# Optimization experiments

Hardware: AMD Instinct MI355X
Metric: run time of the kernel (lower is better)

## Reference

```python
import jax, jax.numpy as jnp
import numpy as np

BS, N1, N2, D = 2, 512, 512, 64  # in_dim = out_dim = D
TEMP = 1.0
EPS = 1e-5
POOL_RATIO = 0.5


def setup_inputs() -> dict:
    key = jax.random.key(0)
    ks = iter(jax.random.split(key, 32))
    nrm = lambda shape, s=0.05: jax.random.normal(next(ks), shape, dtype=jnp.float32) * s
    inp = {
        "x1": jax.random.normal(next(ks), (BS, N1, D), dtype=jnp.float32),
        "x2": jax.random.normal(next(ks), (BS, N2, D), dtype=jnp.float32),
        # proj_type1 / proj_type2 (Linear in->in); weights stored [in, out]
        "W1": nrm((D, D)), "b1": jnp.zeros((D,), jnp.float32),
        "W2": nrm((D, D)), "b2": jnp.zeros((D,), jnp.float32),
        # att_proj / att_projM (Linear in->out)
        "Wa": nrm((D, D)), "ba": jnp.zeros((D,), jnp.float32),
        "WaM": nrm((D, D)), "baM": jnp.zeros((D,), jnp.float32),
        # attention weight vectors (out_dim, 1)
        "w11": nrm((D, 1), 0.2), "w22": nrm((D, 1), 0.2),
        "w12": nrm((D, 1), 0.2), "wM": nrm((D, 1), 0.2),
        # projections
        "Wpa": nrm((D, D)), "bpa": jnp.zeros((D,), jnp.float32),
        "Wwoa": nrm((D, D)), "bwoa": jnp.zeros((D,), jnp.float32),
        "WpaM": nrm((D, D)), "bpaM": jnp.zeros((D,), jnp.float32),
        "WwoaM": nrm((D, D)), "bwoaM": jnp.zeros((D,), jnp.float32),
        # BatchNorm1d affine params
        "gamma": jnp.ones((D,), jnp.float32), "beta": jnp.zeros((D,), jnp.float32),
        # GraphPool score layer (Linear D->1), shared pool as in Model
        "Wp": nrm((D, 1), 0.2), "bp": jnp.zeros((1,), jnp.float32),
    }
    return inp


def _htrg_gat(x1, x2, W1, b1, W2, b2, Wa, ba, WaM, baM, w11, w22, w12, wM,
              Wpa, bpa, Wwoa, bwoa, WpaM, bpaM, WwoaM, bwoaM, gamma, beta):
    n1 = x1.shape[1]
    x1p = x1 @ W1 + b1
    x2p = x2 @ W2 + b2
    x = jnp.concatenate([x1p, x2p], axis=1)          # (b, N, d)
    master = jnp.mean(x, axis=1, keepdims=True)       # (b, 1, d)

    # --- attention map: pairwise node products, blockwise score weights ---
    pair = x[:, :, None, :] * x[:, None, :, :]        # (b, N, N, d)
    t = jnp.tanh(pair @ Wa + ba)                      # (b, N, N, d)
    top = jnp.concatenate([t[:, :n1, :n1] @ w11, t[:, :n1, n1:] @ w12], axis=2)
    bot = jnp.concatenate([t[:, n1:, :n1] @ w12, t[:, n1:, n1:] @ w22], axis=2)
    board = jnp.concatenate([top, bot], axis=1) / TEMP  # (b, N, N, 1)
    att = jax.nn.softmax(board, axis=-2)

    # --- master update ---
    tm = jnp.tanh((x * master) @ WaM + baM)           # (b, N, d)
    am = jax.nn.softmax((tm @ wM) / TEMP, axis=-2)    # (b, N, 1)
    agg_m = jnp.einsum('bn,bnd->bd', am[..., 0], x)[:, None, :]  # (b, 1, d)
    master_new = (agg_m @ WpaM + bpaM) + (master @ WwoaM + bwoaM)

    # --- project nodes with attention ---
    agg = jnp.einsum('bij,bjd->bid', att[..., 0], x)  # (b, N, d)
    xo = (agg @ Wpa + bpa) + (x @ Wwoa + bwoa)

    # --- BatchNorm1d over flattened (b*N) rows, then SELU ---
    mu = jnp.mean(xo, axis=(0, 1))
    var = jnp.var(xo, axis=(0, 1))
    xo = (xo - mu) * jax.lax.rsqrt(var + EPS) * gamma + beta
    xo = jax.nn.selu(xo)
    return xo[:, :n1], xo[:, n1:], master_new


def _graph_pool(x, Wp, bp):
    # scores -> sigmoid -> scale features -> top-k gather
    n = x.shape[1]
    k = max(int(n * POOL_RATIO), 1)
    scores = jax.nn.sigmoid(x @ Wp + bp)              # (b, n, 1)
    _, idx = jax.lax.top_k(scores[..., 0], k)         # (b, k)
    xs = x * scores
    return jnp.take_along_axis(xs, idx[..., None], axis=1)  # (b, k, d)


def reference(x1, x2, W1, b1, W2, b2, Wa, ba, WaM, baM, w11, w22, w12, wM,
              Wpa, bpa, Wwoa, bwoa, WpaM, bpaM, WwoaM, bwoaM, gamma, beta, Wp, bp):
    o1, o2, master = _htrg_gat(x1, x2, W1, b1, W2, b2, Wa, ba, WaM, baM,
                               w11, w22, w12, wM, Wpa, bpa, Wwoa, bwoa,
                               WpaM, bpaM, WwoaM, bwoaM, gamma, beta)
    p1 = _graph_pool(o1, Wp, bp)
    p2 = _graph_pool(o2, Wp, bp)
    return jnp.concatenate([p1, p2], axis=1)          # (b, n1/2 + n2/2, d)
```

## Files before the change

### kernel.cpp

```cpp
#include <hip/hip_runtime.h>

typedef float f32x4 __attribute__((ext_vector_type(4)));
typedef short short8 __attribute__((ext_vector_type(8)));

#define N_TOT 1024
#define N_HALF 512
#define D 64
#define KPOOL 256

#if __has_builtin(__builtin_amdgcn_exp2f)
#define EXP2F(x) __builtin_amdgcn_exp2f(x)
#else
#define EXP2F(x) __expf((x) * 0.6931471805599453f)
#endif
#if __has_builtin(__builtin_amdgcn_rcpf)
#define RCPF(x) __builtin_amdgcn_rcpf(x)
#else
#define RCPF(x) (1.0f / (x))
#endif

__device__ __forceinline__ short f2bf(float v) {
    unsigned u = __float_as_uint(v);
    u += 0x7FFFu + ((u >> 16) & 1u);
    return (short)(u >> 16);
}
__device__ __forceinline__ float bf2f(unsigned short u) {
    return __uint_as_float(((unsigned)u) << 16);
}

__global__ void k_proj(const float* __restrict__ x1, const float* __restrict__ x2,
                       const float* __restrict__ W1, const float* __restrict__ b1,
                       const float* __restrict__ W2, const float* __restrict__ b2,
                       float* __restrict__ x_f, unsigned short* __restrict__ x_bf,
                       unsigned short* __restrict__ xT_hi, unsigned short* __restrict__ xT_lo) {
    int r = blockIdx.x;
    int b = r >> 10, n = r & 1023;
    const float *src, *W, *bias;
    if (n < N_HALF) { src = x1 + (b * N_HALF + n) * D;            W = W1; bias = b1; }
    else            { src = x2 + (b * N_HALF + (n - N_HALF)) * D; W = W2; bias = b2; }
    __shared__ float row[D];
    int t = threadIdx.x;
    row[t] = src[t];
    __syncthreads();
    float acc = bias[t];
#pragma unroll
    for (int d = 0; d < D; ++d) acc = fmaf(row[d], W[d * D + t], acc);
    unsigned short hi = (unsigned short)f2bf(acc);
    unsigned short lo = (unsigned short)f2bf(acc - bf2f(hi));
    x_f[r * D + t] = acc;
    x_bf[r * D + t] = hi;
    xT_hi[((size_t)b * D + t) * N_TOT + n] = hi;
    xT_lo[((size_t)b * D + t) * N_TOT + n] = lo;
}

__global__ void __launch_bounds__(256)
k_score(const float* __restrict__ x_f, const unsigned short* __restrict__ x_bf,
        const float* __restrict__ Wa, const float* __restrict__ ba,
        const float* __restrict__ w11, const float* __restrict__ w22,
        const float* __restrict__ w12, unsigned* __restrict__ Ep) {
    int bid = blockIdx.x;
    int b = (bid >= 2560) ? 1 : 0;
    int m = bid - b * 2560;
    int i, c0;
    if (m < 1024)      { i = m >> 2;                        c0 = m & 3; }
    else if (m < 1792) { int t = m - 1024; i = 256 + t / 3; c0 = t % 3; }
    else if (m < 2304) { int t = m - 1792; i = 512 + (t >> 1); c0 = t & 1; }
    else               { i = 768 + (m - 2304);              c0 = 0; }
    int jt0 = i >> 4;
    int jts = jt0 + (c0 << 4);
    int jte = (jts + 16 < 64) ? (jts + 16) : 64;

    int tid = threadIdx.x;
    int l = tid & 63, wv = tid >> 6;
    int kc = l & 15, dg = l >> 4;

    __shared__ float xi_s[D];
    if (tid < D) xi_s[tid] = x_f[(b * N_TOT + i) * D + tid];
    __syncthreads();

    const float C2 = 2.885390081777927f;
    const float LOG2E = 1.4426950408889634f;

    const float* wTop = (i < N_HALF) ? w11 : w12;
    const float* wBot = (i < N_HALF) ? w12 : w22;

    short8 bfrag[4][2];
    float bac[4], wm2A[4], wm2B[4];
    float wsumA = 0.f, wsumB = 0.f;
#pragma unroll
    for (int kt = 0; kt < 4; ++kt) {
        int kcol = kt * 16 + kc;
        bac[kt] = ba[kcol] * C2;
        float wA = wTop[kcol], wB = wBot[kcol];
        wm2A[kt] = -2.f * wA; wm2B[kt] = -2.f * wB;
        wsumA += wA; wsumB += wB;
#pragma unroll
        for (int mm = 0; mm < 2; ++mm) {
            short8 f;
#pragma unroll
            for (int e = 0; e < 8; ++e) {
                int d = mm * 32 + dg * 8 + e;
                f[e] = f2bf(xi_s[d] * Wa[d * D + kcol]);
            }
            bfrag[kt][mm] = f;
        }
    }

    const unsigned short* xb_b = x_bf + b * N_TOT * D;
    unsigned* Eb = Ep + ((size_t)b << 20);
    for (int jt = jts + wv; jt < jte; jt += 4) {
        const unsigned short* arow = xb_b + (jt * 16 + kc) * D + dg * 8;
        short8 a0 = *reinterpret_cast<const short8*>(arow);
        short8 a1 = *reinterpret_cast<const short8*>(arow + 32);
        f32x4 acc[4];
#pragma unroll
        for (int kt = 0; kt < 4; ++kt) {
            f32x4 z = {0.f, 0.f, 0.f, 0.f};
            z = __builtin_amdgcn_mfma_f32_16x16x32_bf16(a0, bfrag[kt][0], z, 0, 0, 0);
            z = __builtin_amdgcn_mfma_f32_16x16x32_bf16(a1, bfrag[kt][1], z, 0, 0, 0);
            acc[kt] = z;
        }
        bool top = (jt < 32);
        float wsum_t = top ? wsumA : wsumB;
#pragma unroll
        for (int r = 0; r < 4; ++r) {
            float part = wsum_t;
#pragma unroll
            for (int kt = 0; kt < 4; ++kt) {
                float e2 = EXP2F(fmaf(acc[kt][r], C2, bac[kt]));
                float rcv = RCPF(e2 + 1.f);
                part = fmaf(top ? wm2A[kt] : wm2B[kt], rcv, part);
            }
            part += __shfl_xor(part, 1);
            part += __shfl_xor(part, 2);
            part += __shfl_xor(part, 4);
            part += __shfl_xor(part, 8);
            if (kc == 0) {
                int j = jt * 16 + dg * 4 + r;
                if (j >= i) {
                    float e = EXP2F(part * LOG2E);
                    unsigned short eh = (unsigned short)f2bf(e);
                    unsigned short el = (unsigned short)f2bf(e - bf2f(eh));
                    unsigned pk = ((unsigned)eh << 16) | (unsigned)el;
                    Eb[(size_t)i * N_TOT + j] = pk;
                    if (j > i) Eb[(size_t)j * N_TOT + i] = pk;
                }
            }
        }
    }
}

__global__ void __launch_bounds__(256)
k_aggp(const unsigned* __restrict__ Ep,
       const unsigned short* __restrict__ xT_hi, const unsigned short* __restrict__ xT_lo,
       float* __restrict__ pagg, float* __restrict__ rowsum_part) {
    int blk = blockIdx.x;
    int b = blk >> 7, rest = blk & 127;
    int it = rest >> 1, jh = rest & 1;
    int i0 = it * 16, jbase = jh * 512;
    int tid = threadIdx.x;
    int l = tid & 63, wv = tid >> 6;
    int kc = l & 15, dg = l >> 4;

    const unsigned* Eb = Ep + ((size_t)b << 20);
    const unsigned short* xTH = xT_hi + (size_t)b * D * N_TOT;
    const unsigned short* xTL = xT_lo + (size_t)b * D * N_TOT;

    f32x4 C0 = {0.f, 0.f, 0.f, 0.f}, C1 = C0, C2v = C0;
    const unsigned* Ap = Eb + (size_t)(i0 + kc) * N_TOT + jbase + dg * 8;
    const unsigned short* BH = xTH + (size_t)(wv * 16 + kc) * N_TOT + jbase + dg * 8;
    const unsigned short* BL = xTL + (size_t)(wv * 16 + kc) * N_TOT + jbase + dg * 8;
#pragma unroll 4
    for (int ks = 0; ks < 16; ++ks) {
        uint4 p0 = *reinterpret_cast<const uint4*>(Ap + ks * 32);
        uint4 p1 = *reinterpret_cast<const uint4*>(Ap + ks * 32 + 4);
        short8 ah, al;
        ah[0] = (short)(p0.x >> 16); al[0] = (short)(p0.x & 0xffff);
        ah[1] = (short)(p0.y >> 16); al[1] = (short)(p0.y & 0xffff);
        ah[2] = (short)(p0.z >> 16); al[2] = (short)(p0.z & 0xffff);
        ah[3] = (short)(p0.w >> 16); al[3] = (short)(p0.w & 0xffff);
        ah[4] = (short)(p1.x >> 16); al[4] = (short)(p1.x & 0xffff);
        ah[5] = (short)(p1.y >> 16); al[5] = (short)(p1.y & 0xffff);
        ah[6] = (short)(p1.z >> 16); al[6] = (short)(p1.z & 0xffff);
        ah[7] = (short)(p1.w >> 16); al[7] = (short)(p1.w & 0xffff);
        short8 bh = *reinterpret_cast<const short8*>(BH + ks * 32);
        short8 bl = *reinterpret_cast<const short8*>(BL + ks * 32);
        C0 = __builtin_amdgcn_mfma_f32_16x16x32_bf16(ah, bh, C0, 0, 0, 0);
        C1 = __builtin_amdgcn_mfma_f32_16x16x32_bf16(ah, bl, C1, 0, 0, 0);
        C2v = __builtin_amdgcn_mfma_f32_16x16x32_bf16(al, bh, C2v, 0, 0, 0);
    }
    f32x4 C = (C0 + C1) + C2v;

    {
        int row = wv * 4 + (l & 3);
        int seg = l >> 2;
        const unsigned* Er = Eb + (size_t)(i0 + row) * N_TOT + jbase + seg * 32;
        float rs = 0.f;
#pragma unroll
        for (int u = 0; u < 8; ++u) {
            uint4 v = *reinterpret_cast<const uint4*>(Er + u * 4);
            rs += __uint_as_float(v.x & 0xffff0000u) + __uint_as_float(v.x << 16);
            rs += __uint_as_float(v.y & 0xffff0000u) + __uint_as_float(v.y << 16);
            rs += __uint_as_float(v.z & 0xffff0000u) + __uint_as_float(v.z << 16);
            rs += __uint_as_float(v.w & 0xffff0000u) + __uint_as_float(v.w << 16);
        }
        rs += __shfl_xor(rs, 4);
        rs += __shfl_xor(rs, 8);
        rs += __shfl_xor(rs, 16);
        rs += __shfl_xor(rs, 32);
        if ((l & 3) == (l >> 2) % 4 && l < 4)
            ;
        if (l < 4) rowsum_part[(size_t)(b * 2 + jh) * N_TOT + i0 + wv * 4 + l] = rs;
    }

#pragma unroll
    for (int r = 0; r < 4; ++r)
        pagg[((size_t)(b * 2 + jh) * N_TOT + i0 + dg * 4 + r) * D + wv * 16 + kc] = C[r];
}

__global__ void __launch_bounds__(256)
k_aggfin(const float* __restrict__ pagg, const float* __restrict__ rowsum_part,
         const float* __restrict__ x_f,
         const float* __restrict__ Wpa, const float* __restrict__ bpa,
         const float* __restrict__ Wwoa, const float* __restrict__ bwoa,
         float* __restrict__ xo_pre, float* __restrict__ partials) {
    int b = blockIdx.x >> 6, it = blockIdx.x & 63;
    int i0 = it * 16;
    int tid = threadIdx.x;
    int l = tid & 63, wv = tid >> 6;

    __shared__ float aggL[16][D];
    __shared__ float xiL[16][D];
    __shared__ float xoL[16][D];
    __shared__ float riL[16];

    const float* p0 = pagg + ((size_t)(b * 2 + 0) * N_TOT + i0) * D;
    const float* p1 = pagg + ((size_t)(b * 2 + 1) * N_TOT + i0) * D;
    const float* xB = x_f + ((size_t)b * N_TOT + i0) * D;
#pragma unroll
    for (int u = 0; u < 4; ++u) {
        int idx = tid + u * 256;
        reinterpret_cast<float*>(aggL)[idx] = p0[idx] + p1[idx];
        reinterpret_cast<float*>(xiL)[idx] = xB[idx];
    }
    if (tid < 16)
        riL[tid] = 1.f / (rowsum_part[(size_t)(b * 2 + 0) * N_TOT + i0 + tid] +
                          rowsum_part[(size_t)(b * 2 + 1) * N_TOT + i0 + tid]);
    __syncthreads();
#pragma unroll
    for (int u = 0; u < 4; ++u) {
        int idx = tid + u * 256;
        reinterpret_cast<float*>(aggL)[idx] *= riL[idx >> 6];
    }
    __syncthreads();

    int k = l;
    float xo[4];
#pragma unroll
    for (int r = 0; r < 4; ++r) xo[r] = bpa[k] + bwoa[k];
    for (int dd = 0; dd < D; ++dd) {
        float wp = Wpa[dd * D + k], ww = Wwoa[dd * D + k];
#pragma unroll
        for (int r = 0; r < 4; ++r) {
            int row = wv * 4 + r;
            xo[r] += aggL[row][dd] * wp + xiL[row][dd] * ww;
        }
    }
#pragma unroll
    for (int r = 0; r < 4; ++r) {
        int row = wv * 4 + r;
        xo_pre[((size_t)b * N_TOT + i0 + row) * D + k] = xo[r];
        xoL[row][k] = xo[r];
    }
    __syncthreads();
    if (tid < D) {
        float s = 0.f, q = 0.f;
#pragma unroll
        for (int mm = 0; mm < 16; ++mm) { float v = xoL[mm][tid]; s += v; q = fmaf(v, v, q); }
        partials[blockIdx.x * 128 + tid] = s;
        partials[blockIdx.x * 128 + 64 + tid] = q;
    }
}

__global__ void k_stats2(const float* __restrict__ partials, float* __restrict__ stats) {
    int t = threadIdx.x;
    int g = t >> 7;
    int f128 = t & 127;
    float s = 0.f;
    for (int blk = g * 32; blk < g * 32 + 32; ++blk) s += partials[blk * 128 + f128];
    __shared__ float SQ[4][128];
    SQ[g][f128] = s;
    __syncthreads();
    if (t < 128) {
        float tot = SQ[0][t] + SQ[1][t] + SQ[2][t] + SQ[3][t];
        SQ[0][t] = tot;
    }
    __syncthreads();
    if (t < D) {
        float mu = SQ[0][t] * (1.f / 2048.f);
        float ex2 = SQ[0][64 + t] * (1.f / 2048.f);
        stats[t] = mu;
        stats[D + t] = rsqrtf(ex2 - mu * mu + 1e-5f);
    }
}

__global__ void k_norm(const float* __restrict__ xo_pre, const float* __restrict__ stats,
                       const float* __restrict__ gamma, const float* __restrict__ beta,
                       const float* __restrict__ Wp, const float* __restrict__ bp,
                       float* __restrict__ o_norm, float* __restrict__ scores) {
    int r = blockIdx.x * 4 + (threadIdx.x >> 6);
    int t = threadIdx.x & 63;
    float v = xo_pre[r * D + t];
    v = (v - stats[t]) * stats[D + t] * gamma[t] + beta[t];
    const float kScale = 1.0507009873554805f, kAlpha = 1.6732632423543772f;
    v = (v > 0.f) ? kScale * v : kScale * kAlpha * expm1f(v);
    o_norm[r * D + t] = v;
    float pd = v * Wp[t];
#pragma unroll
    for (int off = 32; off >= 1; off >>= 1) pd += __shfl_xor(pd, off);
    if (t == 0) scores[r] = 1.f / (1.f + __expf(-(pd + bp[0])));
}

__global__ void __launch_bounds__(512)
k_pool(const float* __restrict__ o_norm, const float* __restrict__ scores,
       float* __restrict__ out) {
    int b = blockIdx.x >> 1, half = blockIdx.x & 1;
    int tid = threadIdx.x;
    __shared__ float sc_s[N_HALF];
    __shared__ unsigned long long keys[N_HALF];
    __shared__ unsigned short map[KPOOL];

    {
        float sc = scores[b * N_TOT + half * N_HALF + tid];
        sc_s[tid] = sc;
        keys[tid] = ((unsigned long long)__float_as_uint(sc) << 10) | (unsigned)(511 - tid);
    }
    __syncthreads();
    unsigned long long mine = keys[tid];
    int cnt = 0;
#pragma unroll 8
    for (int qq = 0; qq < N_HALF; ++qq) cnt += (keys[qq] > mine) ? 1 : 0;
    if (cnt < KPOOL) map[cnt] = (unsigned short)tid;
    __syncthreads();
    int d = tid & 63;
    for (int rr = tid >> 6; rr < KPOOL; rr += 8) {
        int src = map[rr];
        out[(size_t)(b * N_HALF + half * KPOOL + rr) * D + d] =
            o_norm[(size_t)(b * N_TOT + half * N_HALF + src) * D + d] * sc_s[src];
    }
}

extern "C" void kernel_launch(void* const* d_in, const int* in_sizes, int n_in,
                              void* d_out, int out_size, void* d_ws, size_t ws_size,
                              hipStream_t stream) {
    const float* x1   = (const float*)d_in[0];
    const float* x2   = (const float*)d_in[1];
    const float* W1   = (const float*)d_in[2];
    const float* b1   = (const float*)d_in[3];
    const float* W2   = (const float*)d_in[4];
    const float* b2   = (const float*)d_in[5];
    const float* Wa   = (const float*)d_in[6];
    const float* ba   = (const float*)d_in[7];
    const float* w11  = (const float*)d_in[10];
    const float* w22  = (const float*)d_in[11];
    const float* w12  = (const float*)d_in[12];
    const float* Wpa  = (const float*)d_in[14];
    const float* bpa  = (const float*)d_in[15];
    const float* Wwoa = (const float*)d_in[16];
    const float* bwoa = (const float*)d_in[17];
    const float* gamma= (const float*)d_in[22];
    const float* beta = (const float*)d_in[23];
    const float* Wp   = (const float*)d_in[24];
    const float* bp   = (const float*)d_in[25];
    float* out = (float*)d_out;

    char* ws = (char*)d_ws;
    float*          x_f     = (float*)(ws + 0);
    unsigned short* x_bf    = (unsigned short*)(ws + 524288);
    unsigned short* xT_hi   = (unsigned short*)(ws + 786432);
    unsigned short* xT_lo   = (unsigned short*)(ws + 1048576);
    unsigned*       Ep      = (unsigned*)(ws + 1310720);
    float*          pagg    = (float*)(ws + 9699328);
    float*          rowsum  = (float*)(ws + 10747904);
    float*          xo_pre  = (float*)(ws + 10764288);
    float*          o_norm  = (float*)(ws + 11288576);
    float*          scores  = (float*)(ws + 11812864);
    float*          partials= (float*)(ws + 11821056);
    float*          stats   = (float*)(ws + 11886592);

    hipLaunchKernelGGL(k_proj, dim3(2 * N_TOT), dim3(64), 0, stream,
                       x1, x2, W1, b1, W2, b2, x_f, x_bf, xT_hi, xT_lo);
    hipLaunchKernelGGL(k_score, dim3(5120), dim3(256), 0, stream,
                       x_f, x_bf, Wa, ba, w11, w22, w12, Ep);
    hipLaunchKernelGGL(k_aggp, dim3(256), dim3(256), 0, stream,
                       Ep, xT_hi, xT_lo, pagg, rowsum);
    hipLaunchKernelGGL(k_aggfin, dim3(128), dim3(256), 0, stream,
                       pagg, rowsum, x_f, Wpa, bpa, Wwoa, bwoa, xo_pre, partials);
    hipLaunchKernelGGL(k_stats2, dim3(1), dim3(512), 0, stream, partials, stats);
    hipLaunchKernelGGL(k_norm, dim3(512), dim3(256), 0, stream,
                       xo_pre, stats, gamma, beta, Wp, bp, o_norm, scores);
    hipLaunchKernelGGL(k_pool, dim3(4), dim3(512), 0, stream, o_norm, scores, out);
}
```

Measured before the change: 91.18 us.

## Fuse aggregation kernels, batch projection rows, simplify score block mapping

The projection kernel now computes 8 rows per block, reusing each weight load across them and writing the transposed hi/lo bf16 outputs as vector stores. The score kernel gives one block per row i, covering all upper-triangle tiles, with paired quarter rows reversed to even out load across blocks. This replaces the finer chunked mapping and cuts the block count. The split-K aggregation and its finalize kernel are merged into one kernel that does the full K range, computes the row sums itself, and applies the output projection. This removes the pagg round trip and one launch, but leaves only 128 blocks, each with a longer serial K loop.

```diff
diff --git a/kernel.cpp b/kernel.cpp
--- a/kernel.cpp
+++ b/kernel.cpp
@@ -28,29 +28,47 @@
     return __uint_as_float(((unsigned)u) << 16);
 }
 
-__global__ void k_proj(const float* __restrict__ x1, const float* __restrict__ x2,
-                       const float* __restrict__ W1, const float* __restrict__ b1,
-                       const float* __restrict__ W2, const float* __restrict__ b2,
-                       float* __restrict__ x_f, unsigned short* __restrict__ x_bf,
-                       unsigned short* __restrict__ xT_hi, unsigned short* __restrict__ xT_lo) {
-    int r = blockIdx.x;
-    int b = r >> 10, n = r & 1023;
+__global__ void __launch_bounds__(64)
+k_proj(const float* __restrict__ x1, const float* __restrict__ x2,
+       const float* __restrict__ W1, const float* __restrict__ b1,
+       const float* __restrict__ W2, const float* __restrict__ b2,
+       float* __restrict__ x_f, unsigned short* __restrict__ x_bf,
+       unsigned short* __restrict__ xT_hi, unsigned short* __restrict__ xT_lo) {
+    int blk = blockIdx.x;
+    int b = blk >> 7;
+    int n0 = (blk & 127) * 8;
+    int t = threadIdx.x;
+
     const float *src, *W, *bias;
-    if (n < N_HALF) { src = x1 + (b * N_HALF + n) * D;            W = W1; bias = b1; }
-    else            { src = x2 + (b * N_HALF + (n - N_HALF)) * D; W = W2; bias = b2; }
-    __shared__ float row[D];
-    int t = threadIdx.x;
-    row[t] = src[t];
-    __syncthreads();
-    float acc = bias[t];
-#pragma unroll
-    for (int d = 0; d < D; ++d) acc = fmaf(row[d], W[d * D + t], acc);
-    unsigned short hi = (unsigned short)f2bf(acc);
-    unsigned short lo = (unsigned short)f2bf(acc - bf2f(hi));
-    x_f[r * D + t] = acc;
-    x_bf[r * D + t] = hi;
-    xT_hi[((size_t)b * D + t) * N_TOT + n] = hi;
-    xT_lo[((size_t)b * D + t) * N_TOT + n] = lo;
+    if (n0 < N_HALF) { src = x1 + (b * N_HALF + n0) * D;            W = W1; bias = b1; }
+    else             { src = x2 + (b * N_HALF + (n0 - N_HALF)) * D; W = W2; bias = b2; }
+
+    __shared__ float rows[8][D];
+#pragma unroll
+    for (int r = 0; r < 8; ++r) rows[r][t] = src[r * D + t];
+    __syncthreads();
+
+    float bv = bias[t];
+    float acc[8];
+#pragma unroll
+    for (int r = 0; r < 8; ++r) acc[r] = bv;
+    for (int d = 0; d < D; ++d) {
+        float w = W[d * D + t];
+#pragma unroll
+        for (int r = 0; r < 8; ++r) acc[r] = fmaf(rows[r][d], w, acc[r]);
+    }
+
+    short8 hiv, lov;
+#pragma unroll
+    for (int r = 0; r < 8; ++r) {
+        unsigned short hi = (unsigned short)f2bf(acc[r]);
+        unsigned short lo = (unsigned short)f2bf(acc[r] - bf2f(hi));
+        x_f[((size_t)b * N_TOT + n0 + r) * D + t] = acc[r];
+        x_bf[((size_t)b * N_TOT + n0 + r) * D + t] = hi;
+        hiv[r] = (short)hi; lov[r] = (short)lo;
+    }
+    *reinterpret_cast<short8*>(xT_hi + ((size_t)b * D + t) * N_TOT + n0) = hiv;
+    *reinterpret_cast<short8*>(xT_lo + ((size_t)b * D + t) * N_TOT + n0) = lov;
 }
 
 __global__ void __launch_bounds__(256)
@@ -59,17 +77,9 @@
         const float* __restrict__ w11, const float* __restrict__ w22,
         const float* __restrict__ w12, unsigned* __restrict__ Ep) {
     int bid = blockIdx.x;
-    int b = (bid >= 2560) ? 1 : 0;
-    int m = bid - b * 2560;
-    int i, c0;
-    if (m < 1024)      { i = m >> 2;                        c0 = m & 3; }
-    else if (m < 1792) { int t = m - 1024; i = 256 + t / 3; c0 = t % 3; }
-    else if (m < 2304) { int t = m - 1792; i = 512 + (t >> 1); c0 = t & 1; }
-    else               { i = 768 + (m - 2304);              c0 = 0; }
-    int jt0 = i >> 4;
-    int jts = jt0 + (c0 << 4);
-    int jte = (jts + 16 < 64) ? (jts + 16) : 64;
-
+    int b = bid >> 10, n = bid & 1023;
+    int q = n >> 8, c = n & 255;
+    int i = (q << 8) | ((q & 1) ? (255 - c) : c);
     int tid = threadIdx.x;
     int l = tid & 63, wv = tid >> 6;
     int kc = l & 15, dg = l >> 4;
@@ -108,7 +118,8 @@
 
     const unsigned short* xb_b = x_bf + b * N_TOT * D;
     unsigned* Eb = Ep + ((size_t)b << 20);
-    for (int jt = jts + wv; jt < jte; jt += 4) {
+    int jt0 = i >> 4;
+    for (int jt = jt0 + wv; jt < 64; jt += 4) {
         const unsigned short* arow = xb_b + (jt * 16 + kc) * D + dg * 8;
         short8 a0 = *reinterpret_cast<const short8*>(arow);
         short8 a1 = *reinterpret_cast<const short8*>(arow + 32);
@@ -151,13 +162,14 @@
 }
 
 __global__ void __launch_bounds__(256)
-k_aggp(const unsigned* __restrict__ Ep,
-       const unsigned short* __restrict__ xT_hi, const unsigned short* __restrict__ xT_lo,
-       float* __restrict__ pagg, float* __restrict__ rowsum_part) {
-    int blk = blockIdx.x;
-    int b = blk >> 7, rest = blk & 127;
-    int it = rest >> 1, jh = rest & 1;
-    int i0 = it * 16, jbase = jh * 512;
+k_agg(const unsigned* __restrict__ Ep,
+      const unsigned short* __restrict__ xT_hi, const unsigned short* __restrict__ xT_lo,
+      const float* __restrict__ x_f,
+      const float* __restrict__ Wpa, const float* __restrict__ bpa,
+      const float* __restrict__ Wwoa, const float* __restrict__ bwoa,
+      float* __restrict__ xo_pre, float* __restrict__ partials) {
+    int b = blockIdx.x >> 6, it = blockIdx.x & 63;
+    int i0 = it * 16;
     int tid = threadIdx.x;
     int l = tid & 63, wv = tid >> 6;
     int kc = l & 15, dg = l >> 4;
@@ -166,12 +178,37 @@
     const unsigned short* xTH = xT_hi + (size_t)b * D * N_TOT;
     const unsigned short* xTL = xT_lo + (size_t)b * D * N_TOT;
 
+    __shared__ float aggL[16][D];
+    __shared__ float xiL[16][D];
+    __shared__ float xoL[16][D];
+    __shared__ float riL[16];
+
+    {
+        int row = wv * 4 + (l & 3);
+        int seg = l >> 2;
+        const unsigned* Er = Eb + (size_t)(i0 + row) * N_TOT + seg * 64;
+        float rs = 0.f;
+#pragma unroll
+        for (int u = 0; u < 16; ++u) {
+            uint4 v = *reinterpret_cast<const uint4*>(Er + u * 4);
+            rs += __uint_as_float(v.x & 0xffff0000u) + __uint_as_float(v.x << 16);
+            rs += __uint_as_float(v.y & 0xffff0000u) + __uint_as_float(v.y << 16);
+            rs += __uint_as_float(v.z & 0xffff0000u) + __uint_as_float(v.z << 16);
+            rs += __uint_as_float(v.w & 0xffff0000u) + __uint_as_float(v.w << 16);
+        }
+        rs += __shfl_xor(rs, 4);
+        rs += __shfl_xor(rs, 8);
+        rs += __shfl_xor(rs, 16);
+        rs += __shfl_xor(rs, 32);
+        if (l < 4) riL[wv * 4 + l] = 1.f / rs;
+    }
+
     f32x4 C0 = {0.f, 0.f, 0.f, 0.f}, C1 = C0, C2v = C0;
-    const unsigned* Ap = Eb + (size_t)(i0 + kc) * N_TOT + jbase + dg * 8;
-    const unsigned short* BH = xTH + (size_t)(wv * 16 + kc) * N_TOT + jbase + dg * 8;
-    const unsigned short* BL = xTL + (size_t)(wv * 16 + kc) * N_TOT + jbase + dg * 8;
+    const unsigned* Ap = Eb + (size_t)(i0 + kc) * N_TOT + dg * 8;
+    const unsigned short* BH = xTH + (size_t)(wv * 16 + kc) * N_TOT + dg * 8;
+    const unsigned short* BL = xTL + (size_t)(wv * 16 + kc) * N_TOT + dg * 8;
 #pragma unroll 4
-    for (int ks = 0; ks < 16; ++ks) {
+    for (int ks = 0; ks < 32; ++ks) {
         uint4 p0 = *reinterpret_cast<const uint4*>(Ap + ks * 32);
         uint4 p1 = *reinterpret_cast<const uint4*>(Ap + ks * 32 + 4);
         short8 ah, al;
@@ -192,66 +229,15 @@
     f32x4 C = (C0 + C1) + C2v;
 
     {
-        int row = wv * 4 + (l & 3);
-        int seg = l >> 2;
-        const unsigned* Er = Eb + (size_t)(i0 + row) * N_TOT + jbase + seg * 32;
-        float rs = 0.f;
-#pragma unroll
-        for (int u = 0; u < 8; ++u) {
-            uint4 v = *reinterpret_cast<const uint4*>(Er + u * 4);
-            rs += __uint_as_float(v.x & 0xffff0000u) + __uint_as_float(v.x << 16);
-            rs += __uint_as_float(v.y & 0xffff0000u) + __uint_as_float(v.y << 16);
-            rs += __uint_as_float(v.z & 0xffff0000u) + __uint_as_float(v.z << 16);
-            rs += __uint_as_float(v.w & 0xffff0000u) + __uint_as_float(v.w << 16);
-        }
-        rs += __shfl_xor(rs, 4);
-        rs += __shfl_xor(rs, 8);
-        rs += __shfl_xor(rs, 16);
-        rs += __shfl_xor(rs, 32);
-        if ((l & 3) == (l >> 2) % 4 && l < 4)
-            ;
-        if (l < 4) rowsum_part[(size_t)(b * 2 + jh) * N_TOT + i0 + wv * 4 + l] = rs;
-    }
+        int row = tid >> 4, quad = tid & 15;
+        const f32x4* xf4 = reinterpret_cast<const f32x4*>(x_f + ((size_t)b * N_TOT + i0) * D);
+        reinterpret_cast<f32x4*>(xiL)[row * 16 + quad] = xf4[row * 16 + quad];
+    }
+    __syncthreads();
 
 #pragma unroll
     for (int r = 0; r < 4; ++r)
-        pagg[((size_t)(b * 2 + jh) * N_TOT + i0 + dg * 4 + r) * D + wv * 16 + kc] = C[r];
-}
-
-__global__ void __launch_bounds__(256)
-k_aggfin(const float* __restrict__ pagg, const float* __restrict__ rowsum_part,
-         const float* __restrict__ x_f,
-         const float* __restrict__ Wpa, const float* __restrict__ bpa,
-         const float* __restrict__ Wwoa, const float* __restrict__ bwoa,
-         float* __restrict__ xo_pre, float* __restrict__ partials) {
-    int b = blockIdx.x >> 6, it = blockIdx.x & 63;
-    int i0 = it * 16;
-    int tid = threadIdx.x;
-    int l = tid & 63, wv = tid >> 6;
-
-    __shared__ float aggL[16][D];
-    __shared__ float xiL[16][D];
-    __shared__ float xoL[16][D];
-    __shared__ float riL[16];
-
-    const float* p0 = pagg + ((size_t)(b * 2 + 0) * N_TOT + i0) * D;
-    const float* p1 = pagg + ((size_t)(b * 2 + 1) * N_TOT + i0) * D;
-    const float* xB = x_f + ((size_t)b * N_TOT + i0) * D;
-#pragma unroll
-    for (int u = 0; u < 4; ++u) {
-        int idx = tid + u * 256;
-        reinterpret_cast<float*>(aggL)[idx] = p0[idx] + p1[idx];
-        reinterpret_cast<float*>(xiL)[idx] = xB[idx];
-    }
-    if (tid < 16)
-        riL[tid] = 1.f / (rowsum_part[(size_t)(b * 2 + 0) * N_TOT + i0 + tid] +
-                          rowsum_part[(size_t)(b * 2 + 1) * N_TOT + i0 + tid]);
-    __syncthreads();
-#pragma unroll
-    for (int u = 0; u < 4; ++u) {
-        int idx = tid + u * 256;
-        reinterpret_cast<float*>(aggL)[idx] *= riL[idx >> 6];
-    }
+        aggL[dg * 4 + r][wv * 16 + kc] = C[r] * riL[dg * 4 + r];
     __syncthreads();
 
     int k = l;
@@ -274,11 +260,11 @@
     }
     __syncthreads();
     if (tid < D) {
-        float s = 0.f, q = 0.f;
-#pragma unroll
-        for (int mm = 0; mm < 16; ++mm) { float v = xoL[mm][tid]; s += v; q = fmaf(v, v, q); }
+        float s = 0.f, qv = 0.f;
+#pragma unroll
+        for (int mm = 0; mm < 16; ++mm) { float v = xoL[mm][tid]; s += v; qv = fmaf(v, v, qv); }
         partials[blockIdx.x * 128 + tid] = s;
-        partials[blockIdx.x * 128 + 64 + tid] = q;
+        partials[blockIdx.x * 128 + 64 + tid] = qv;
     }
 }
 
@@ -380,22 +366,18 @@
     unsigned short* xT_hi   = (unsigned short*)(ws + 786432);
     unsigned short* xT_lo   = (unsigned short*)(ws + 1048576);
     unsigned*       Ep      = (unsigned*)(ws + 1310720);
-    float*          pagg    = (float*)(ws + 9699328);
-    float*          rowsum  = (float*)(ws + 10747904);
-    float*          xo_pre  = (float*)(ws + 10764288);
-    float*          o_norm  = (float*)(ws + 11288576);
-    float*          scores  = (float*)(ws + 11812864);
-    float*          partials= (float*)(ws + 11821056);
-    float*          stats   = (float*)(ws + 11886592);
-
-    hipLaunchKernelGGL(k_proj, dim3(2 * N_TOT), dim3(64), 0, stream,
+    float*          xo_pre  = (float*)(ws + 9699328);
+    float*          o_norm  = (float*)(ws + 10223616);
+    float*          scores  = (float*)(ws + 10747904);
+    float*          partials= (float*)(ws + 10756096);
+    float*          stats   = (float*)(ws + 10821632);
+
+    hipLaunchKernelGGL(k_proj, dim3(256), dim3(64), 0, stream,
                        x1, x2, W1, b1, W2, b2, x_f, x_bf, xT_hi, xT_lo);
-    hipLaunchKernelGGL(k_score, dim3(5120), dim3(256), 0, stream,
+    hipLaunchKernelGGL(k_score, dim3(2048), dim3(256), 0, stream,
                        x_f, x_bf, Wa, ba, w11, w22, w12, Ep);
-    hipLaunchKernelGGL(k_aggp, dim3(256), dim3(256), 0, stream,
-                       Ep, xT_hi, xT_lo, pagg, rowsum);
-    hipLaunchKernelGGL(k_aggfin, dim3(128), dim3(256), 0, stream,
-                       pagg, rowsum, x_f, Wpa, bpa, Wwoa, bwoa, xo_pre, partials);
+    hipLaunchKernelGGL(k_agg, dim3(128), dim3(256), 0, stream,
+                       Ep, xT_hi, xT_lo, x_f, Wpa, bpa, Wwoa, bwoa, xo_pre, partials);
     hipLaunchKernelGGL(k_stats2, dim3(1), dim3(512), 0, stream, partials, stats);
     hipLaunchKernelGGL(k_norm, dim3(512), dim3(256), 0, stream,
                        xo_pre, stats, gamma, beta, Wp, bp, o_norm, scores);
```

Result: slower. 93.73 us (+2.8%).

## Pair mirrored rows per score block and batch four rows per projection block

Applied to the files above, without the earlier changes.

The score kernel now gives each block two rows, i and N-1-i, which together cover a constant number of upper-triangle tiles. This replaces the old 5120-block grid with fragmented chunks by 1024 balanced blocks, cutting per-block setup (the B fragment build) and giving even work per block. The projection kernel now handles four rows per block so each W load is reused across rows, and it writes the transposed hi/lo outputs as 4-wide vector stores. In exchange there are fewer blocks, so less parallelism, and each score block runs longer serial work.

```diff
diff --git a/kernel.cpp b/kernel.cpp
--- a/kernel.cpp
+++ b/kernel.cpp
@@ -2,6 +2,7 @@
 
 typedef float f32x4 __attribute__((ext_vector_type(4)));
 typedef short short8 __attribute__((ext_vector_type(8)));
+typedef short s16x4 __attribute__((ext_vector_type(4)));
 
 #define N_TOT 1024
 #define N_HALF 512
@@ -28,29 +29,47 @@
     return __uint_as_float(((unsigned)u) << 16);
 }
 
-__global__ void k_proj(const float* __restrict__ x1, const float* __restrict__ x2,
-                       const float* __restrict__ W1, const float* __restrict__ b1,
-                       const float* __restrict__ W2, const float* __restrict__ b2,
-                       float* __restrict__ x_f, unsigned short* __restrict__ x_bf,
-                       unsigned short* __restrict__ xT_hi, unsigned short* __restrict__ xT_lo) {
-    int r = blockIdx.x;
-    int b = r >> 10, n = r & 1023;
+__global__ void __launch_bounds__(64)
+k_proj(const float* __restrict__ x1, const float* __restrict__ x2,
+       const float* __restrict__ W1, const float* __restrict__ b1,
+       const float* __restrict__ W2, const float* __restrict__ b2,
+       float* __restrict__ x_f, unsigned short* __restrict__ x_bf,
+       unsigned short* __restrict__ xT_hi, unsigned short* __restrict__ xT_lo) {
+    int blk = blockIdx.x;
+    int b = blk >> 8;
+    int n0 = (blk & 255) * 4;
+    int t = threadIdx.x;
+
     const float *src, *W, *bias;
-    if (n < N_HALF) { src = x1 + (b * N_HALF + n) * D;            W = W1; bias = b1; }
-    else            { src = x2 + (b * N_HALF + (n - N_HALF)) * D; W = W2; bias = b2; }
-    __shared__ float row[D];
-    int t = threadIdx.x;
-    row[t] = src[t];
-    __syncthreads();
-    float acc = bias[t];
-#pragma unroll
-    for (int d = 0; d < D; ++d) acc = fmaf(row[d], W[d * D + t], acc);
-    unsigned short hi = (unsigned short)f2bf(acc);
-    unsigned short lo = (unsigned short)f2bf(acc - bf2f(hi));
-    x_f[r * D + t] = acc;
-    x_bf[r * D + t] = hi;
-    xT_hi[((size_t)b * D + t) * N_TOT + n] = hi;
-    xT_lo[((size_t)b * D + t) * N_TOT + n] = lo;
+    if (n0 < N_HALF) { src = x1 + (b * N_HALF + n0) * D;            W = W1; bias = b1; }
+    else             { src = x2 + (b * N_HALF + (n0 - N_HALF)) * D; W = W2; bias = b2; }
+
+    __shared__ float rows[4][D];
+#pragma unroll
+    for (int r = 0; r < 4; ++r) rows[r][t] = src[r * D + t];
+    __syncthreads();
+
+    float bv = bias[t];
+    float acc[4];
+#pragma unroll
+    for (int r = 0; r < 4; ++r) acc[r] = bv;
+    for (int d = 0; d < D; ++d) {
+        float w = W[d * D + t];
+#pragma unroll
+        for (int r = 0; r < 4; ++r) acc[r] = fmaf(rows[r][d], w, acc[r]);
+    }
+
+    s16x4 hiv, lov;
+#pragma unroll
+    for (int r = 0; r < 4; ++r) {
+        unsigned short hi = (unsigned short)f2bf(acc[r]);
+        unsigned short lo = (unsigned short)f2bf(acc[r] - bf2f(hi));
+        x_f[((size_t)b * N_TOT + n0 + r) * D + t] = acc[r];
+        x_bf[((size_t)b * N_TOT + n0 + r) * D + t] = hi;
+        hiv[r] = (short)hi; lov[r] = (short)lo;
+    }
+    *reinterpret_cast<s16x4*>(xT_hi + ((size_t)b * D + t) * N_TOT + n0) = hiv;
+    *reinterpret_cast<s16x4*>(xT_lo + ((size_t)b * D + t) * N_TOT + n0) = lov;
 }
 
 __global__ void __launch_bounds__(256)
@@ -59,91 +78,89 @@
         const float* __restrict__ w11, const float* __restrict__ w22,
         const float* __restrict__ w12, unsigned* __restrict__ Ep) {
     int bid = blockIdx.x;
-    int b = (bid >= 2560) ? 1 : 0;
-    int m = bid - b * 2560;
-    int i, c0;
-    if (m < 1024)      { i = m >> 2;                        c0 = m & 3; }
-    else if (m < 1792) { int t = m - 1024; i = 256 + t / 3; c0 = t % 3; }
-    else if (m < 2304) { int t = m - 1792; i = 512 + (t >> 1); c0 = t & 1; }
-    else               { i = 768 + (m - 2304);              c0 = 0; }
-    int jt0 = i >> 4;
-    int jts = jt0 + (c0 << 4);
-    int jte = (jts + 16 < 64) ? (jts + 16) : 64;
-
+    int b = bid >> 9, c = bid & 511;
     int tid = threadIdx.x;
     int l = tid & 63, wv = tid >> 6;
     int kc = l & 15, dg = l >> 4;
 
-    __shared__ float xi_s[D];
-    if (tid < D) xi_s[tid] = x_f[(b * N_TOT + i) * D + tid];
-    __syncthreads();
-
     const float C2 = 2.885390081777927f;
     const float LOG2E = 1.4426950408889634f;
 
-    const float* wTop = (i < N_HALF) ? w11 : w12;
-    const float* wBot = (i < N_HALF) ? w12 : w22;
-
-    short8 bfrag[4][2];
-    float bac[4], wm2A[4], wm2B[4];
-    float wsumA = 0.f, wsumB = 0.f;
-#pragma unroll
-    for (int kt = 0; kt < 4; ++kt) {
-        int kcol = kt * 16 + kc;
-        bac[kt] = ba[kcol] * C2;
-        float wA = wTop[kcol], wB = wBot[kcol];
-        wm2A[kt] = -2.f * wA; wm2B[kt] = -2.f * wB;
-        wsumA += wA; wsumB += wB;
-#pragma unroll
-        for (int mm = 0; mm < 2; ++mm) {
-            short8 f;
-#pragma unroll
-            for (int e = 0; e < 8; ++e) {
-                int d = mm * 32 + dg * 8 + e;
-                f[e] = f2bf(xi_s[d] * Wa[d * D + kcol]);
-            }
-            bfrag[kt][mm] = f;
-        }
-    }
-
+    __shared__ float xi_s[D];
     const unsigned short* xb_b = x_bf + b * N_TOT * D;
     unsigned* Eb = Ep + ((size_t)b << 20);
-    for (int jt = jts + wv; jt < jte; jt += 4) {
-        const unsigned short* arow = xb_b + (jt * 16 + kc) * D + dg * 8;
-        short8 a0 = *reinterpret_cast<const short8*>(arow);
-        short8 a1 = *reinterpret_cast<const short8*>(arow + 32);
-        f32x4 acc[4];
+
+#pragma unroll
+    for (int phase = 0; phase < 2; ++phase) {
+        int i = phase ? (N_TOT - 1 - c) : c;
+
+        __syncthreads();
+        if (tid < D) xi_s[tid] = x_f[(b * N_TOT + i) * D + tid];
+        __syncthreads();
+
+        const float* wTop = (i < N_HALF) ? w11 : w12;
+        const float* wBot = (i < N_HALF) ? w12 : w22;
+
+        short8 bfrag[4][2];
+        float bac[4], wm2A[4], wm2B[4];
+        float wsumA = 0.f, wsumB = 0.f;
 #pragma unroll
         for (int kt = 0; kt < 4; ++kt) {
-            f32x4 z = {0.f, 0.f, 0.f, 0.f};
-            z = __builtin_amdgcn_mfma_f32_16x16x32_bf16(a0, bfrag[kt][0], z, 0, 0, 0);
-            z = __builtin_amdgcn_mfma_f32_16x16x32_bf16(a1, bfrag[kt][1], z, 0, 0, 0);
-            acc[kt] = z;
+            int kcol = kt * 16 + kc;
+            bac[kt] = ba[kcol] * C2;
+            float wA = wTop[kcol], wB = wBot[kcol];
+            wm2A[kt] = -2.f * wA; wm2B[kt] = -2.f * wB;
+            wsumA += wA; wsumB += wB;
+#pragma unroll
+            for (int mm = 0; mm < 2; ++mm) {
+                short8 f;
+#pragma unroll
+                for (int e = 0; e < 8; ++e) {
+                    int d = mm * 32 + dg * 8 + e;
+                    f[e] = f2bf(xi_s[d] * Wa[d * D + kcol]);
+                }
+                bfrag[kt][mm] = f;
+            }
         }
-        bool top = (jt < 32);
-        float wsum_t = top ? wsumA : wsumB;
-#pragma unroll
-        for (int r = 0; r < 4; ++r) {
-            float part = wsum_t;
+
+        int jt0 = i >> 4;
+        for (int jt = jt0 + wv; jt < 64; jt += 4) {
+            const unsigned short* arow = xb_b + (jt * 16 + kc) * D + dg * 8;
+            short8 a0 = *reinterpret_cast<const short8*>(arow);
+            short8 a1 = *reinterpret_cast<const short8*>(arow + 32);
+            f32x4 acc[4];
 #pragma unroll
             for (int kt = 0; kt < 4; ++kt) {
-                float e2 = EXP2F(fmaf(acc[kt][r], C2, bac[kt]));
-                float rcv = RCPF(e2 + 1.f);
-                part = fmaf(top ? wm2A[kt] : wm2B[kt], rcv, part);
+                f32x4 z = {0.f, 0.f, 0.f, 0.f};
+                z = __builtin_amdgcn_mfma_f32_16x16x32_bf16(a0, bfrag[kt][0], z, 0, 0, 0);
+                z = __builtin_amdgcn_mfma_f32_16x16x32_bf16(a1, bfrag[kt][1], z, 0, 0, 0);
+                acc[kt] = z;
             }
-            part += __shfl_xor(part, 1);
-            part += __shfl_xor(part, 2);
-            part += __shfl_xor(part, 4);
-            part += __shfl_xor(part, 8);
-            if (kc == 0) {
-                int j = jt * 16 + dg * 4 + r;
-                if (j >= i) {
-                    float e = EXP2F(part * LOG2E);
-                    unsigned short eh = (unsigned short)f2bf(e);
-                    unsigned short el = (unsigned short)f2bf(e - bf2f(eh));
-                    unsigned pk = ((unsigned)eh << 16) | (unsigned)el;
-                    Eb[(size_t)i * N_TOT + j] = pk;
-                    if (j > i) Eb[(size_t)j * N_TOT + i] = pk;
+            bool top = (jt < 32);
+            float wsum_t = top ? wsumA : wsumB;
+#pragma unroll
+            for (int r = 0; r < 4; ++r) {
+                float part = wsum_t;
+#pragma unroll
+                for (int kt = 0; kt < 4; ++kt) {
+                    float e2 = EXP2F(fmaf(acc[kt][r], C2, bac[kt]));
+                    float rcv = RCPF(e2 + 1.f);
+                    part = fmaf(top ? wm2A[kt] : wm2B[kt], rcv, part);
+                }
+                part += __shfl_xor(part, 1);
+                part += __shfl_xor(part, 2);
+                part += __shfl_xor(part, 4);
+                part += __shfl_xor(part, 8);
+                if (kc == 0) {
+                    int j = jt * 16 + dg * 4 + r;
+                    if (j >= i) {
+                        float e = EXP2F(part * LOG2E);
+                        unsigned short eh = (unsigned short)f2bf(e);
+                        unsigned short el = (unsigned short)f2bf(e - bf2f(eh));
+                        unsigned pk = ((unsigned)eh << 16) | (unsigned)el;
+                        Eb[(size_t)i * N_TOT + j] = pk;
+                        if (j > i) Eb[(size_t)j * N_TOT + i] = pk;
+                    }
                 }
             }
         }
@@ -208,8 +225,6 @@
         rs += __shfl_xor(rs, 8);
         rs += __shfl_xor(rs, 16);
         rs += __shfl_xor(rs, 32);
-        if ((l & 3) == (l >> 2) % 4 && l < 4)
-            ;
         if (l < 4) rowsum_part[(size_t)(b * 2 + jh) * N_TOT + i0 + wv * 4 + l] = rs;
     }
 
@@ -274,11 +289,11 @@
     }
     __syncthreads();
     if (tid < D) {
-        float s = 0.f, q = 0.f;
-#pragma unroll
-        for (int mm = 0; mm < 16; ++mm) { float v = xoL[mm][tid]; s += v; q = fmaf(v, v, q); }
+        float s = 0.f, qv = 0.f;
+#pragma unroll
+        for (int mm = 0; mm < 16; ++mm) { float v = xoL[mm][tid]; s += v; qv = fmaf(v, v, qv); }
         partials[blockIdx.x * 128 + tid] = s;
-        partials[blockIdx.x * 128 + 64 + tid] = q;
+        partials[blockIdx.x * 128 + 64 + tid] = qv;
     }
 }
 
@@ -388,9 +403,9 @@
     float*          partials= (float*)(ws + 11821056);
     float*          stats   = (float*)(ws + 11886592);
 
-    hipLaunchKernelGGL(k_proj, dim3(2 * N_TOT), dim3(64), 0, stream,
+    hipLaunchKernelGGL(k_proj, dim3(512), dim3(64), 0, stream,
                        x1, x2, W1, b1, W2, b2, x_f, x_bf, xT_hi, xT_lo);
-    hipLaunchKernelGGL(k_score, dim3(5120), dim3(256), 0, stream,
+    hipLaunchKernelGGL(k_score, dim3(1024), dim3(256), 0, stream,
                        x_f, x_bf, Wa, ba, w11, w22, w12, Ep);
     hipLaunchKernelGGL(k_aggp, dim3(256), dim3(256), 0, stream,
                        Ep, xT_hi, xT_lo, pagg, rowsum);
```

After: 98.46 us. 8.0% more time.
